# Performance work log

Hardware: AMD Instinct MI355X
Metric: run time of the kernel (lower is better)

Reference implementation:

```python
import jax, jax.numpy as jnp
import numpy as np

NUM_BINS = 10
NUM_CLASSES = 100
BATCH = 1_000_000


def setup_inputs() -> dict:
    key = jax.random.key(0)
    k1, k2 = jax.random.split(key)
    outputs = jax.random.normal(k1, (BATCH, NUM_CLASSES), dtype=jnp.float32)
    targets = jax.random.randint(k2, (BATCH,), 0, NUM_CLASSES, dtype=jnp.int64)
    return {"outputs": outputs, "targets": targets}


def reference(outputs, targets):
    """Expected Calibration Error, single-pass histogram formulation.

    Faithful to the torch module: confidence = softmax prob of the TRUE class,
    bins are half-open (b_i, b_{i+1}] over linspace(0,1,n_bins+1); p==0 falls
    in no bin (excluded, matching the torch loop).
    """
    n_bins = NUM_BINS
    probs = jax.nn.softmax(outputs, axis=1)                  # [N, C]
    N = outputs.shape[0]
    targets = targets.astype(jnp.int32)
    true_class_probs = probs[jnp.arange(N), targets]         # [N]
    pred = jnp.argmax(probs, axis=1).astype(jnp.int32)       # [N]
    correct = (pred == targets).astype(probs.dtype)          # [N]

    # bin i covers (boundaries[i], boundaries[i+1]]; searchsorted 'left' gives
    # insertion idx j with boundaries[j-1] < p <= boundaries[j]  ->  bin = j-1.
    boundaries = jnp.linspace(0.0, 1.0, n_bins + 1)
    bin_idx = jnp.searchsorted(boundaries, true_class_probs, side="left") - 1
    valid = bin_idx >= 0                                     # p == 0 excluded
    bin_idx = jnp.clip(bin_idx, 0, n_bins - 1)
    w = valid.astype(probs.dtype)

    counts = jax.ops.segment_sum(w, bin_idx, num_segments=n_bins)
    sum_prob = jax.ops.segment_sum(true_class_probs * w, bin_idx, num_segments=n_bins)
    sum_corr = jax.ops.segment_sum(correct * w, bin_idx, num_segments=n_bins)

    nonempty = counts > 0
    denom = jnp.where(nonempty, counts, 1.0)
    avg_prob = sum_prob / denom
    accuracy = sum_corr / denom
    ece = jnp.sum(jnp.where(nonempty, counts * jnp.abs(avg_prob - accuracy), 0.0))
    total = jnp.sum(counts)
    return jnp.where(total > 0, ece / jnp.maximum(total, 1.0), 0.0)
```

## Files before the change

kernel.cpp:

```cpp
#include <hip/hip_runtime.h>
#include <math.h>

#define NB 10
#define NCLS 100

__global__ __launch_bounds__(256) void ece_main(const float* __restrict__ outputs,
                                                const int* __restrict__ targets,
                                                double* __restrict__ gacc,
                                                int nrows) {
    __shared__ float s_cnt[NB], s_sp[NB], s_sc[NB];
    const int tid = threadIdx.x;
    if (tid < NB) { s_cnt[tid] = 0.f; s_sp[tid] = 0.f; s_sc[tid] = 0.f; }
    __syncthreads();

    const int lane = tid & 63;
    const int wid  = tid >> 6;
    const int q = lane & 3;
    const int g = lane >> 2;
    const int gwave  = blockIdx.x * 4 + wid;
    const int nwaves = gridDim.x * 4;
    const int ntiles = (nrows + 15) >> 4;

    const float NEG_INF = -__builtin_inff();

    for (int tile = gwave; tile < ntiles; tile += nwaves) {
        const int row = tile * 16 + g;
        const bool active = row < nrows;

        float4 v[6];
        float tail;
        int t;
        if (active) {
            const float* __restrict__ R = outputs + (size_t)row * NCLS;
            #pragma unroll
            for (int k = 0; k < 6; ++k)
                v[k] = *reinterpret_cast<const float4*>(R + q * 4 + k * 16);
            tail = R[96 + q];
            t = targets[row];
        } else {
            #pragma unroll
            for (int k = 0; k < 6; ++k) v[k].x = v[k].y = v[k].z = v[k].w = NEG_INF;
            tail = NEG_INF;
            t = -1;
        }

        float m = v[0].x;
        int   c = q * 4;
        #pragma unroll
        for (int k = 0; k < 6; ++k) {
            const int base = k * 16 + q * 4;
            if (k > 0 && v[k].x > m) { m = v[k].x; c = base; }
            if (v[k].y > m) { m = v[k].y; c = base + 1; }
            if (v[k].z > m) { m = v[k].z; c = base + 2; }
            if (v[k].w > m) { m = v[k].w; c = base + 3; }
        }
        if (tail > m) { m = tail; c = 96 + q; }

        #pragma unroll
        for (int off = 1; off <= 2; off <<= 1) {
            const float om = __shfl_xor(m, off);
            const int   oc = __shfl_xor(c, off);
            if (om > m || (om == m && oc < c)) { m = om; c = oc; }
        }

        float s = 0.f, te = 0.f;
        #pragma unroll
        for (int k = 0; k < 6; ++k) {
            const int base = k * 16 + q * 4;
            const float e0 = __expf(v[k].x - m);
            const float e1 = __expf(v[k].y - m);
            const float e2 = __expf(v[k].z - m);
            const float e3 = __expf(v[k].w - m);
            s += (e0 + e1) + (e2 + e3);
            if (base     == t) te = e0;
            if (base + 1 == t) te = e1;
            if (base + 2 == t) te = e2;
            if (base + 3 == t) te = e3;
        }
        {
            const float et = __expf(tail - m);
            s += et;
            if (96 + q == t) te = et;
        }
        #pragma unroll
        for (int off = 1; off <= 2; off <<= 1) {
            s  += __shfl_xor(s, off);
            te += __shfl_xor(te, off);
        }

        if (q == 0 && active) {
            const float p = te / s;
            const float corr = (c == t) ? 1.0f : 0.0f;
            const float b[NB + 1] = {0.0f, 0.1f, 0.2f, 0.3f, 0.4f, 0.5f,
                                     0.6f, 0.7f, 0.8f, 0.9f, 1.0f};
            int j = 0;
            #pragma unroll
            for (int k = 0; k <= NB; ++k) j += (b[k] < p) ? 1 : 0;
            int bin = j - 1;
            if (bin >= 0) {
                if (bin > NB - 1) bin = NB - 1;
                atomicAdd(&s_cnt[bin], 1.0f);
                atomicAdd(&s_sp[bin], p);
                atomicAdd(&s_sc[bin], corr);
            }
        }
    }

    __syncthreads();
    if (tid < NB) {
        atomicAdd(&gacc[tid],          (double)s_cnt[tid]);
        atomicAdd(&gacc[NB + tid],     (double)s_sp[tid]);
        atomicAdd(&gacc[2 * NB + tid], (double)s_sc[tid]);
    }
}

__global__ void ece_final(const double* __restrict__ gacc, float* __restrict__ out) {
    if (threadIdx.x == 0 && blockIdx.x == 0) {
        double ece = 0.0, total = 0.0;
        for (int i = 0; i < NB; ++i) {
            const double c = gacc[i];
            if (c > 0.0) {
                const double ap = gacc[NB + i] / c;
                const double ac = gacc[2 * NB + i] / c;
                ece += c * fabs(ap - ac);
                total += c;
            }
        }
        out[0] = (total > 0.0) ? (float)(ece / total) : 0.0f;
    }
}

extern "C" void kernel_launch(void* const* d_in, const int* in_sizes, int n_in,
                              void* d_out, int out_size, void* d_ws, size_t ws_size,
                              hipStream_t stream) {
    const float* outputs = (const float*)d_in[0];
    const int*   targets = (const int*)d_in[1];
    float* out   = (float*)d_out;
    double* gacc = (double*)d_ws;

    const int nrows = in_sizes[1];

    hipMemsetAsync(gacc, 0, 3 * NB * sizeof(double), stream);

    const int blocks = 2048;
    ece_main<<<blocks, 256, 0, stream>>>(outputs, targets, gacc, nrows);
    ece_final<<<1, 64, 0, stream>>>(gacc, out);
}
```

Before: 113.8 us.

## Stage row tiles through shared memory with coalesced float4 loads

Each block now loads a contiguous 64-row tile of logits into padded shared memory, along with its targets, using fully coalesced float4 reads. It then computes softmax, argmax and binning from LDS instead of strided per-row global reads. This targets the scattered 64-byte segments each quad previously fetched at a 400-byte row stride. In exchange it adds two block-wide barriers per tile and does no double buffering, so load and compute no longer overlap within a block. It also needs about 27KB of LDS per block.

```diff
diff --git a/kernel.cpp b/kernel.cpp
--- a/kernel.cpp
+++ b/kernel.cpp
@@ -3,46 +3,58 @@
 
 #define NB 10
 #define NCLS 100
+#define RPT 64
+#define LSTR 104
 
 __global__ __launch_bounds__(256) void ece_main(const float* __restrict__ outputs,
                                                 const int* __restrict__ targets,
                                                 double* __restrict__ gacc,
                                                 int nrows) {
+    __shared__ float tile[RPT * LSTR];
+    __shared__ int   ttgt[RPT];
     __shared__ float s_cnt[NB], s_sp[NB], s_sc[NB];
+
     const int tid = threadIdx.x;
     if (tid < NB) { s_cnt[tid] = 0.f; s_sp[tid] = 0.f; s_sc[tid] = 0.f; }
-    __syncthreads();
 
-    const int lane = tid & 63;
-    const int wid  = tid >> 6;
-    const int q = lane & 3;
-    const int g = lane >> 2;
-    const int gwave  = blockIdx.x * 4 + wid;
-    const int nwaves = gridDim.x * 4;
-    const int ntiles = (nrows + 15) >> 4;
+    const int r_loc = tid >> 2;
+    const int q     = tid & 3;
 
-    const float NEG_INF = -__builtin_inff();
+    const int ntiles = (nrows + RPT - 1) / RPT;
 
-    for (int tile = gwave; tile < ntiles; tile += nwaves) {
-        const int row = tile * 16 + g;
+    for (int ti = blockIdx.x; ti < ntiles; ti += gridDim.x) {
+        const int row0 = ti * RPT;
+        const int nr   = min(nrows - row0, RPT);
+        const int fmax = nr * 25;
+
+        __syncthreads();
+        {
+            const float4* __restrict__ src =
+                reinterpret_cast<const float4*>(outputs + (size_t)row0 * NCLS);
+            #pragma unroll
+            for (int k = 0; k < 7; ++k) {
+                const int f = tid + 256 * k;
+                if (f < fmax) {
+                    const float4 v = src[f];
+                    const int pr = f / 25;
+                    const int pc = (f % 25) * 4;
+                    *reinterpret_cast<float4*>(&tile[pr * LSTR + pc]) = v;
+                }
+            }
+            if (tid < nr) ttgt[tid] = targets[row0 + tid];
+        }
+        __syncthreads();
+
+        const int  row    = row0 + r_loc;
         const bool active = row < nrows;
 
+        const float* __restrict__ L = &tile[r_loc * LSTR];
         float4 v[6];
-        float tail;
-        int t;
-        if (active) {
-            const float* __restrict__ R = outputs + (size_t)row * NCLS;
-            #pragma unroll
-            for (int k = 0; k < 6; ++k)
-                v[k] = *reinterpret_cast<const float4*>(R + q * 4 + k * 16);
-            tail = R[96 + q];
-            t = targets[row];
-        } else {
-            #pragma unroll
-            for (int k = 0; k < 6; ++k) v[k].x = v[k].y = v[k].z = v[k].w = NEG_INF;
-            tail = NEG_INF;
-            t = -1;
-        }
+        #pragma unroll
+        for (int k = 0; k < 6; ++k)
+            v[k] = *reinterpret_cast<const float4*>(&L[q * 4 + k * 16]);
+        const float tail = L[96 + q];
+        const int t = ttgt[r_loc & (RPT - 1)];
 
         float m = v[0].x;
         int   c = q * 4;
```

After: 146.5 us. +28.7%, slower.
